# Kernel optimization log

Hardware: AMD Instinct MI355X
Metric: run time of the kernel (lower is better)

The kernel has to match this reference:

```python
import jax, jax.numpy as jnp
import numpy as np

GRID = (32, 32)          # 448 // 14
IMG = (448, 448)
SIGMA = 4.0              # anomalib AnomalyMapGenerator default smoothing


def _l2norm(x, axis=-1, eps=1e-12):
    return x / jnp.clip(jnp.linalg.norm(x, axis=axis, keepdims=True), eps, None)


def _gaussian_blur(x, sigma=SIGMA):
    # kornia-style: kernel_size = 2*int(4*sigma+0.5)+1, reflect padding, separable conv
    radius = int(4.0 * sigma + 0.5)
    t = jnp.arange(-radius, radius + 1, dtype=x.dtype)
    k = jnp.exp(-0.5 * (t / sigma) ** 2)
    k = k / k.sum()
    xp = jnp.pad(x, ((0, 0), (0, 0), (radius, radius), (radius, radius)), mode='reflect')
    kh = k.reshape(1, 1, -1, 1)
    kw = k.reshape(1, 1, 1, -1)
    dn = ('NCHW', 'OIHW', 'NCHW')
    y = jax.lax.conv_general_dilated(xp, kh, (1, 1), 'VALID', dimension_numbers=dn)
    return jax.lax.conv_general_dilated(y, kw, (1, 1), 'VALID', dimension_numbers=dn)


def setup_inputs() -> dict:
    key = jax.random.key(0)
    k1, k2 = jax.random.split(key)
    features = jax.random.normal(k1, (8, 1024, 384), dtype=jnp.float32)
    memory_bank = jax.random.normal(k2, (65536, 384), dtype=jnp.float32)
    return {"features": features, "memory_bank": memory_bank}


def reference(features, memory_bank):
    # features: (B, N, D) patch tokens from DINOv2; memory_bank: (M, D)
    b, n, _ = features.shape
    f = _l2norm(features)                 # F.normalize(features, p=2, dim=1) on flattened patches
    mb = _l2norm(memory_bank)             # bank stores normalized embeddings
    sim = jnp.einsum('bnd,md->bnm', f, mb)            # (B, N, M) cosine similarity
    dists = jnp.clip(1.0 - sim, 0.0, 2.0)
    min_dists = dists.min(axis=2)                     # k = num_neighbours = 1 -> row min
    num_top = max(int(n * 0.01), 1)
    top_vals = jax.lax.top_k(min_dists, num_top)[0]
    pred_score = top_vals.mean(axis=1, keepdims=True) # (B, 1)
    amap = min_dists.reshape(b, 1, *GRID)
    amap = jax.image.resize(amap, (b, 1, *IMG), method='bilinear')
    anomaly_map = _gaussian_blur(amap)                # (B, 1, H, W)
    return pred_score, anomaly_map
```

## Files before the change

### kernel.cpp

```cpp
#include <hip/hip_runtime.h>
#include <hip/hip_bf16.h>

#define NROW_F 8192
#define NROW_B 65536
#define KDIM   384
#define BM 256
#define BN 256
#define NSUB 8
#define NGRP (NROW_B / (BN * NSUB))
#define NBM  (NROW_F / BM)
#define NWG  (NBM * NGRP)

#define LDSA 0
#define LDSB 98304
#define LDSS 147456
#define LDSR 98304
#define LDS_TOT 155648

typedef int   i32x4 __attribute__((ext_vector_type(4)));
typedef float f32x4 __attribute__((ext_vector_type(4)));

static __device__ __forceinline__ void stage16(const void* g, void* l) {
  __builtin_amdgcn_global_load_lds(
      (const __attribute__((address_space(1))) unsigned int*)g,
      (__attribute__((address_space(3))) unsigned int*)l, 16, 0, 0);
}

__global__ __launch_bounds__(256) void quantize_rows_kernel(
    const float* __restrict__ in, char* __restrict__ out8,
    float* __restrict__ scales, int nrows) {
  int row  = blockIdx.x * 4 + (threadIdx.x >> 6);
  int lane = threadIdx.x & 63;
  if (row >= nrows) return;
  const float* r = in + (size_t)row * KDIM;
  float v[6];
  float ss = 0.f, mx = 0.f;
#pragma unroll
  for (int i = 0; i < 6; ++i) {
    v[i] = r[lane + i * 64];
    ss += v[i] * v[i];
    mx = fmaxf(mx, fabsf(v[i]));
  }
#pragma unroll
  for (int d = 1; d < 64; d <<= 1) {
    ss += __shfl_xor(ss, d, 64);
    mx = fmaxf(mx, __shfl_xor(mx, d, 64));
  }
  mx = fmaxf(mx, 1e-30f);
  float inv = rsqrtf(fmaxf(ss, 1e-24f));
  float scl = 127.0f / mx;
  if (lane == 0) scales[row] = mx * inv * (1.0f / 127.0f);
  char* o = out8 + (size_t)row * KDIM;
#pragma unroll
  for (int i = 0; i < 6; ++i)
    o[lane + i * 64] = (char)__float2int_rn(v[i] * scl);
}

__global__ __launch_bounds__(512) void maxsim_kernel(
    const char* __restrict__ F8,
    const char* __restrict__ B8,
    const float* __restrict__ sA,
    const float* __restrict__ sB,
    float* __restrict__ partial) {
  __shared__ __align__(16) char smem[LDS_TOT];

  const int tid  = threadIdx.x;
  const int wv   = tid >> 6;
  const int lane = tid & 63;
  const int l15  = lane & 15;
  const int lhi  = lane >> 4;
  const int wr   = wv >> 2;
  const int wc   = wv & 3;

  const int wg  = (blockIdx.x & 7) * (NWG / 8) + (blockIdx.x >> 3);
  const int bm  = wg & (NBM - 1);
  const int grp = wg >> 5;
  const size_t brow = (size_t)bm * BM;

  const int srow16 = lane >> 2;
  const int gsw    = (lane & 3) ^ ((lane >> 3) & 3);

  {
    const char* gA = F8 + ((size_t)(brow + wv * 32 + srow16)) * KDIM + gsw * 16;
    char* lA = smem + LDSA + wv * 2048;
#pragma unroll
    for (int kt = 0; kt < 6; ++kt) {
      stage16(gA + kt * 64,              lA + kt * 16384);
      stage16(gA + kt * 64 + 16 * KDIM,  lA + kt * 16384 + 1024);
    }
  }
  stage16((const char*)(sB + (size_t)grp * 2048) + wv * 1024 + lane * 16,
          smem + LDSS + wv * 1024);

  auto stageB = [&](int kt, int buf) {
    const char* g = B8 + ((size_t)grp * 2048 + (kt / 6) * 256 + wv * 32 + srow16) * KDIM
                    + (kt % 6) * 64 + gsw * 16;
    char* l = smem + LDSB + buf * 16384 + wv * 2048;
    stage16(g, l);
    stage16(g + 16 * KDIM, l + 1024);
  };
  stageB(0, 0);
  stageB(1, 1);

  const int cof = ((l15 >> 1) & 3) << 4;

  auto ldA8 = [&](int k6, int m) -> i32x4 {
    int byte = k6 * 16384 + (wr * 128 + m * 16 + l15) * 64 + ((lhi << 4) ^ cof);
    return *reinterpret_cast<const i32x4*>(smem + LDSA + byte);
  };
  auto ldB8 = [&](int buf, int n) -> i32x4 {
    int byte = buf * 16384 + (wc * 64 + n * 16 + l15) * 64 + ((lhi << 4) ^ cof);
    return *reinterpret_cast<const i32x4*>(smem + LDSB + byte);
  };

  i32x4 acc[8][4];
  f32x4 vm[8];
#pragma unroll
  for (int m = 0; m < 8; ++m) {
    vm[m] = f32x4{-1e30f, -1e30f, -1e30f, -1e30f};
#pragma unroll
    for (int n = 0; n < 4; ++n) acc[m][n] = i32x4{0, 0, 0, 0};
  }

  for (int sub = 0; sub < NSUB; ++sub) {
#pragma unroll
    for (int k6 = 0; k6 < 6; ++k6) {
      const int kt = sub * 6 + k6;
      stageB((kt + 2) % (NSUB * 6), (k6 + 2) % 3);
      asm volatile("s_waitcnt vmcnt(4)" ::: "memory");
      __builtin_amdgcn_s_barrier();

      i32x4 a[8], b[4];
#pragma unroll
      for (int m = 0; m < 8; ++m) a[m] = ldA8(k6, m);
#pragma unroll
      for (int n = 0; n < 4; ++n) b[n] = ldB8(k6 % 3, n);
      asm volatile("s_waitcnt lgkmcnt(0)" ::: "memory");
      __builtin_amdgcn_s_setprio(1);
#pragma unroll
      for (int n = 0; n < 4; ++n)
#pragma unroll
        for (int m = 0; m < 8; ++m)
          acc[m][n] = __builtin_amdgcn_mfma_i32_16x16x64_i8(a[m], b[n], acc[m][n], 0, 0, 0);
      __builtin_amdgcn_s_setprio(0);
      asm volatile("" ::: "memory");
      __builtin_amdgcn_s_barrier();
    }
    float sb[4];
#pragma unroll
    for (int n = 0; n < 4; ++n)
      sb[n] = *reinterpret_cast<const float*>(
          smem + LDSS + (sub * 256 + wc * 64 + n * 16 + l15) * 4);
#pragma unroll
    for (int m = 0; m < 8; ++m) {
#pragma unroll
      for (int n = 0; n < 4; ++n)
#pragma unroll
        for (int j = 0; j < 4; ++j)
          vm[m][j] = fmaxf(vm[m][j], (float)acc[m][n][j] * sb[n]);
#pragma unroll
      for (int n = 0; n < 4; ++n) acc[m][n] = i32x4{0, 0, 0, 0};
    }
  }

  asm volatile("s_waitcnt vmcnt(0)" ::: "memory");
#pragma unroll
  for (int d = 1; d < 16; d <<= 1)
#pragma unroll
    for (int m = 0; m < 8; ++m)
#pragma unroll
      for (int j = 0; j < 4; ++j)
        vm[m][j] = fmaxf(vm[m][j], __shfl_xor(vm[m][j], d, 64));

  float* red = (float*)(smem + LDSR);
  __syncthreads();
  if (l15 == 0) {
#pragma unroll
    for (int m = 0; m < 8; ++m)
#pragma unroll
      for (int j = 0; j < 4; ++j)
        red[wc * 256 + wr * 128 + m * 16 + lhi * 4 + j] = vm[m][j];
  }
  __syncthreads();
  if (tid < 256) {
    float x = fmaxf(fmaxf(red[tid], red[256 + tid]),
                    fmaxf(red[512 + tid], red[768 + tid]));
    partial[(size_t)grp * NROW_F + brow + tid] = x * sA[brow + tid];
  }
}

__global__ __launch_bounds__(256) void combine_kernel(
    const float* __restrict__ partial, float* __restrict__ md) {
  int r = blockIdx.x * 256 + threadIdx.x;
  if (r >= NROW_F) return;
  float m = -1e30f;
#pragma unroll
  for (int c = 0; c < NGRP; ++c) m = fmaxf(m, partial[(size_t)c * NROW_F + r]);
  float d = 1.0f - m;
  d = fminf(fmaxf(d, 0.0f), 2.0f);
  md[r] = d;
}

__global__ __launch_bounds__(256) void topk_kernel(
    const float* __restrict__ md, float* __restrict__ out) {
  __shared__ float buf[1024];
  __shared__ float svals[256];
  __shared__ int   sidx[256];
  int b = blockIdx.x, tid = threadIdx.x;
  for (int i = tid; i < 1024; i += 256) buf[i] = md[b * 1024 + i];
  __syncthreads();
  float total = 0.f;
  for (int it = 0; it < 10; ++it) {
    float best = -1e30f; int bi = 0;
    for (int i = tid; i < 1024; i += 256)
      if (buf[i] > best) { best = buf[i]; bi = i; }
    svals[tid] = best; sidx[tid] = bi;
    __syncthreads();
    for (int s = 128; s > 0; s >>= 1) {
      if (tid < s && svals[tid + s] > svals[tid]) {
        svals[tid] = svals[tid + s]; sidx[tid] = sidx[tid + s];
      }
      __syncthreads();
    }
    if (tid == 0) { total += svals[0]; buf[sidx[0]] = -1e30f; }
    __syncthreads();
  }
  if (tid == 0) out[b] = total * 0.1f;
}

__global__ __launch_bounds__(256) void build_w_kernel(float* __restrict__ W) {
  int idx = blockIdx.x * 256 + threadIdx.x;
  if (idx >= 448 * 32) return;
  int y = idx >> 5, g = idx & 31;
  float ksum = 0.f, acc = 0.f;
#pragma unroll
  for (int t = -16; t <= 16; ++t) {
    float ft = (float)t * 0.25f;
    float kv = expf(-0.5f * ft * ft);
    ksum += kv;
    int p = y + t;
    p = (p < 0) ? -p : ((p > 447) ? 894 - p : p);
    float src = ((float)p + 0.5f) * (1.0f / 14.0f) - 0.5f;
    float fl = floorf(src);
    int i0 = (int)fl;
    float fr = src - fl;
    int c0 = i0 < 0 ? 0 : (i0 > 31 ? 31 : i0);
    int i1 = i0 + 1;
    int c1 = i1 < 0 ? 0 : (i1 > 31 ? 31 : i1);
    float w = 0.f;
    if (c0 == g) w += 1.0f - fr;
    if (c1 == g) w += fr;
    acc += kv * w;
  }
  W[idx] = acc / ksum;
}

__global__ __launch_bounds__(256) void map_stage1_kernel(
    const float* __restrict__ md, const float* __restrict__ W,
    float* __restrict__ tmp) {
  int idx = blockIdx.x * 256 + threadIdx.x;
  if (idx >= 8 * 448 * 32) return;
  int gx = idx & 31;
  int y  = (idx >> 5) % 448;
  int b  = idx / (448 * 32);
  const float* w = W + y * 32;
  const float* m = md + b * 1024 + gx;
  float s = 0.f;
#pragma unroll
  for (int gy = 0; gy < 32; ++gy) s += w[gy] * m[gy * 32];
  tmp[idx] = s;
}

__global__ __launch_bounds__(256) void map_stage2_kernel(
    const float* __restrict__ tmp, const float* __restrict__ W,
    float* __restrict__ out) {
  int idx = blockIdx.x * 256 + threadIdx.x;
  if (idx >= 8 * 448 * 448) return;
  int x    = idx % 448;
  int ypos = idx / 448;
  const float* w = W + x * 32;
  const float* t = tmp + ypos * 32;
  float s = 0.f;
#pragma unroll
  for (int gx = 0; gx < 32; ++gx) s += w[gx] * t[gx];
  out[idx] = s;
}

extern "C" void kernel_launch(void* const* d_in, const int* in_sizes, int n_in,
                              void* d_out, int out_size, void* d_ws, size_t ws_size,
                              hipStream_t stream) {
  const float* features = (const float*)d_in[0];
  const float* bank     = (const float*)d_in[1];
  float* out = (float*)d_out;

  char* ws = (char*)d_ws;
  char*  mb8     = ws;
  char*  f8      = ws + 25165824;
  float* sB      = (float*)(ws + 28311552);
  float* sA      = (float*)(ws + 28573696);
  float* partial = (float*)(ws + 28606464);
  float* md      = (float*)(ws + 29655040);
  float* W       = (float*)(ws + 29687808);
  float* tmp     = (float*)(ws + 29745152);

  quantize_rows_kernel<<<NROW_B / 4, 256, 0, stream>>>(bank, mb8, sB, NROW_B);
  quantize_rows_kernel<<<NROW_F / 4, 256, 0, stream>>>(features, f8, sA, NROW_F);
  maxsim_kernel<<<NWG, 512, 0, stream>>>(f8, mb8, sA, sB, partial);
  combine_kernel<<<NROW_F / 256, 256, 0, stream>>>(partial, md);
  topk_kernel<<<8, 256, 0, stream>>>(md, out);
  build_w_kernel<<<(448 * 32 + 255) / 256, 256, 0, stream>>>(W);
  map_stage1_kernel<<<(8 * 448 * 32 + 255) / 256, 256, 0, stream>>>(md, W, tmp);
  map_stage2_kernel<<<(8 * 448 * 448 + 255) / 256, 256, 0, stream>>>(tmp, W, out + 8);
}
```

Before: 259.2 us.

## Use 16 waves per workgroup in int8 maxsim and move B prefetch after MFMAs

```diff
diff --git a/kernel.cpp b/kernel.cpp
--- a/kernel.cpp
+++ b/kernel.cpp
@@ -56,7 +56,7 @@
     o[lane + i * 64] = (char)__float2int_rn(v[i] * scl);
 }
 
-__global__ __launch_bounds__(512) void maxsim_kernel(
+__global__ __launch_bounds__(1024) void maxsim_kernel(
     const char* __restrict__ F8,
     const char* __restrict__ B8,
     const float* __restrict__ sA,
@@ -77,35 +77,32 @@
   const int grp = wg >> 5;
   const size_t brow = (size_t)bm * BM;
 
-  const int srow16 = lane >> 2;
-  const int gsw    = (lane & 3) ^ ((lane >> 3) & 3);
+  const int srow = tid >> 2;
+  const int gsw  = (tid & 3) ^ ((tid >> 3) & 3);
 
   {
-    const char* gA = F8 + ((size_t)(brow + wv * 32 + srow16)) * KDIM + gsw * 16;
-    char* lA = smem + LDSA + wv * 2048;
-#pragma unroll
-    for (int kt = 0; kt < 6; ++kt) {
-      stage16(gA + kt * 64,              lA + kt * 16384);
-      stage16(gA + kt * 64 + 16 * KDIM,  lA + kt * 16384 + 1024);
-    }
-  }
-  stage16((const char*)(sB + (size_t)grp * 2048) + wv * 1024 + lane * 16,
-          smem + LDSS + wv * 1024);
-
-  auto stageB = [&](int kt, int buf) {
-    const char* g = B8 + ((size_t)grp * 2048 + (kt / 6) * 256 + wv * 32 + srow16) * KDIM
-                    + (kt % 6) * 64 + gsw * 16;
-    char* l = smem + LDSB + buf * 16384 + wv * 2048;
-    stage16(g, l);
-    stage16(g + 16 * KDIM, l + 1024);
+    const char* gA = F8 + (size_t)(brow + srow) * KDIM + gsw * 16;
+    char* lA = smem + LDSA + wv * 1024;
+#pragma unroll
+    for (int kt = 0; kt < 6; ++kt)
+      stage16(gA + kt * 64, lA + kt * 16384);
+  }
+  if (wv < 8)
+    stage16((const char*)(sB + (size_t)grp * 2048) + tid * 16,
+            smem + LDSS + wv * 1024);
+
+  auto stageB = [&](int s2, int koff, int buf) {
+    const char* g = B8 + ((size_t)grp * 2048 + s2 * 256 + srow) * KDIM
+                    + koff * 64 + gsw * 16;
+    stage16(g, smem + LDSB + buf * 16384 + wv * 1024);
   };
-  stageB(0, 0);
-  stageB(1, 1);
+  stageB(0, 0, 0);
+  stageB(0, 1, 1);
 
   const int cof = ((l15 >> 1) & 3) << 4;
 
   auto ldA8 = [&](int k6, int m) -> i32x4 {
-    int byte = k6 * 16384 + (wr * 128 + m * 16 + l15) * 64 + ((lhi << 4) ^ cof);
+    int byte = k6 * 16384 + (wr * 64 + m * 16 + l15) * 64 + ((lhi << 4) ^ cof);
     return *reinterpret_cast<const i32x4*>(smem + LDSA + byte);
   };
   auto ldB8 = [&](int buf, int n) -> i32x4 {
@@ -113,37 +110,42 @@
     return *reinterpret_cast<const i32x4*>(smem + LDSB + byte);
   };
 
-  i32x4 acc[8][4];
-  f32x4 vm[8];
-#pragma unroll
-  for (int m = 0; m < 8; ++m) {
+  i32x4 acc[4][4];
+  f32x4 vm[4];
+#pragma unroll
+  for (int m = 0; m < 4; ++m) {
     vm[m] = f32x4{-1e30f, -1e30f, -1e30f, -1e30f};
 #pragma unroll
     for (int n = 0; n < 4; ++n) acc[m][n] = i32x4{0, 0, 0, 0};
   }
 
+  asm volatile("s_waitcnt vmcnt(1)" ::: "memory");
+  __builtin_amdgcn_s_barrier();
+
   for (int sub = 0; sub < NSUB; ++sub) {
 #pragma unroll
     for (int k6 = 0; k6 < 6; ++k6) {
-      const int kt = sub * 6 + k6;
-      stageB((kt + 2) % (NSUB * 6), (k6 + 2) % 3);
-      asm volatile("s_waitcnt vmcnt(4)" ::: "memory");
-      __builtin_amdgcn_s_barrier();
-
-      i32x4 a[8], b[4];
-#pragma unroll
-      for (int m = 0; m < 8; ++m) a[m] = ldA8(k6, m);
+      i32x4 a[4], b[4];
+#pragma unroll
+      for (int m = 0; m < 4; ++m) a[m] = ldA8(k6, m);
 #pragma unroll
       for (int n = 0; n < 4; ++n) b[n] = ldB8(k6 % 3, n);
       asm volatile("s_waitcnt lgkmcnt(0)" ::: "memory");
+      __builtin_amdgcn_sched_barrier(0);
       __builtin_amdgcn_s_setprio(1);
 #pragma unroll
       for (int n = 0; n < 4; ++n)
 #pragma unroll
-        for (int m = 0; m < 8; ++m)
-          acc[m][n] = __builtin_amdgcn_mfma_i32_16x16x64_i8(a[m], b[n], acc[m][n], 0, 0, 0);
+        for (int m = 0; m < 4; ++m)
+          acc[m][n] = __builtin_amdgcn_mfma_i32_16x16x64_i8(
+              a[m], b[n], acc[m][n], 0, 0, 0);
       __builtin_amdgcn_s_setprio(0);
-      asm volatile("" ::: "memory");
+      {
+        const int s2   = (k6 < 4) ? sub : ((sub + 1) & 7);
+        const int koff = (k6 + 2) % 6;
+        stageB(s2, koff, (k6 + 2) % 3);
+      }
+      asm volatile("s_waitcnt vmcnt(1)" ::: "memory");
       __builtin_amdgcn_s_barrier();
     }
     float sb[4];
@@ -152,7 +154,7 @@
       sb[n] = *reinterpret_cast<const float*>(
           smem + LDSS + (sub * 256 + wc * 64 + n * 16 + l15) * 4);
 #pragma unroll
-    for (int m = 0; m < 8; ++m) {
+    for (int m = 0; m < 4; ++m) {
 #pragma unroll
       for (int n = 0; n < 4; ++n)
 #pragma unroll
@@ -167,7 +169,7 @@
 #pragma unroll
   for (int d = 1; d < 16; d <<= 1)
 #pragma unroll
-    for (int m = 0; m < 8; ++m)
+    for (int m = 0; m < 4; ++m)
 #pragma unroll
       for (int j = 0; j < 4; ++j)
         vm[m][j] = fmaxf(vm[m][j], __shfl_xor(vm[m][j], d, 64));
@@ -176,10 +178,10 @@
   __syncthreads();
   if (l15 == 0) {
 #pragma unroll
-    for (int m = 0; m < 8; ++m)
+    for (int m = 0; m < 4; ++m)
 #pragma unroll
       for (int j = 0; j < 4; ++j)
-        red[wc * 256 + wr * 128 + m * 16 + lhi * 4 + j] = vm[m][j];
+        red[wc * 256 + wr * 64 + m * 16 + lhi * 4 + j] = vm[m][j];
   }
   __syncthreads();
   if (tid < 256) {
@@ -305,7 +307,7 @@
 
   quantize_rows_kernel<<<NROW_B / 4, 256, 0, stream>>>(bank, mb8, sB, NROW_B);
   quantize_rows_kernel<<<NROW_F / 4, 256, 0, stream>>>(features, f8, sA, NROW_F);
-  maxsim_kernel<<<NWG, 512, 0, stream>>>(f8, mb8, sA, sB, partial);
+  maxsim_kernel<<<NWG, 1024, 0, stream>>>(f8, mb8, sA, sB, partial);
   combine_kernel<<<NROW_F / 256, 256, 0, stream>>>(partial, md);
   topk_kernel<<<8, 256, 0, stream>>>(md, out);
   build_w_kernel<<<(448 * 32 + 255) / 256, 256, 0, stream>>>(W);
```

New measurement: 275.3 us. 6.2% more time.
